# Optimization experiments

Measured on AMD Instinct MI355X. Metric: run time of the kernel, lower is better.

## Reference

```python
import jax, jax.numpy as jnp
import numpy as np

N_NODES = 100000
N_EDGES = 1600000
F_IN = 512    # args.in_channels (original node feature dim)
F_GNN = 128   # GCNConv output / 'in_channels' ctor arg
HID = 64
Z_DIM = 64
N_GRAPHS = 512


def setup_inputs() -> dict:
    key = jax.random.key(0)
    ks = jax.random.split(key, 20)
    x = jax.random.normal(ks[0], (N_NODES, F_IN), dtype=jnp.float32)
    edge_index = jax.random.randint(ks[1], (2, N_EDGES), 0, N_NODES)
    batch = jnp.sort(jax.random.randint(ks[2], (N_NODES,), 0, N_GRAPHS))
    eps = jax.random.normal(ks[3], (N_GRAPHS, Z_DIM), dtype=jnp.float32)

    def lin(k, fi, fo):
        # xavier_uniform weight, zero bias
        lim = float(np.sqrt(6.0 / (fi + fo)))
        W = jax.random.uniform(k, (fi, fo), minval=-lim, maxval=lim, dtype=jnp.float32)
        return W, jnp.zeros((fo,), dtype=jnp.float32)

    Wg, bg = lin(ks[4], F_IN, F_GNN)
    We1, be1 = lin(ks[5], 2 * F_GNN, HID)
    We2, be2 = lin(ks[6], HID, HID)
    We3, be3 = lin(ks[7], HID, 2 * Z_DIM)
    Wd1, bd1 = lin(ks[8], Z_DIM, HID)
    Wd2, bd2 = lin(ks[9], HID, HID)
    Wd3, bd3 = lin(ks[10], HID, F_GNN)
    return {"x": x, "edge_index": edge_index, "batch": batch, "eps": eps,
            "Wg": Wg, "bg": bg,
            "We1": We1, "be1": be1, "We2": We2, "be2": be2, "We3": We3, "be3": be3,
            "Wd1": Wd1, "bd1": bd1, "Wd2": Wd2, "bd2": bd2, "Wd3": Wd3, "bd3": bd3}


def _gcn_conv(x, edge_index, Wg, bg):
    # PyG GCNConv: add self-loops, symmetric deg normalization, linear-then-aggregate
    n = x.shape[0]
    loops = jnp.arange(n)
    src = jnp.concatenate([edge_index[0], loops])
    dst = jnp.concatenate([edge_index[1], loops])
    deg = jax.ops.segment_sum(jnp.ones_like(dst, dtype=x.dtype), dst, num_segments=n)
    dinv = jnp.where(deg > 0, jax.lax.rsqrt(jnp.maximum(deg, 1.0)), 0.0)
    norm = dinv[src] * dinv[dst]              # [E+N]
    xw = x @ Wg                               # [N, F_GNN]
    msg = xw[src] * norm[:, None]             # gather + scale: [E+N, F_GNN]
    agg = jax.ops.segment_sum(msg, dst, num_segments=n)
    return agg + bg


def _forward(x, edge_index, batch, eps,
             Wg, bg, We1, be1, We2, be2, We3, be3,
             Wd1, bd1, Wd2, bd2, Wd3, bd3):
    n = x.shape[0]
    g = eps.shape[0]
    # single GNN layer (num_layers=1, JK='last'); dropout omitted (eval determinism)
    node_x = jax.nn.relu(_gcn_conv(x, edge_index, Wg, bg))  # [N, F_GNN]
    # global mean / max pool by graph id
    ones = jnp.ones((n,), dtype=node_x.dtype)
    cnt = jax.ops.segment_sum(ones, batch, num_segments=g)
    mean_p = jax.ops.segment_sum(node_x, batch, num_segments=g) / jnp.maximum(cnt, 1.0)[:, None]
    max_p = jax.ops.segment_max(node_x, batch, num_segments=g)
    graph_x = jnp.concatenate([mean_p, max_p], axis=1)      # [G, 2*F_GNN]
    # gaussian encoder MLP
    t = jax.nn.elu(graph_x @ We1 + be1)
    t = jnp.tanh(t @ We2 + be2)
    ml = t @ We3 + be3
    mu, logvar = jnp.split(ml, 2, axis=1)
    # reparameterise (note: module returns stddev in the 'logvar' slot)
    stddev = 1e-6 + jax.nn.softplus(logvar)
    z = mu + eps * stddev
    # bernoulli decoder MLP
    d = jnp.tanh(z @ Wd1 + bd1)
    d = jax.nn.elu(d @ Wd2 + bd2)
    y = jax.nn.sigmoid(d @ Wd3 + bd3)
    y = jnp.clip(y, 1e-8, 1.0 - 1e-8)
    return mu, stddev, y


def reference(x, edge_index, batch, eps,
              Wg, bg, We1, be1, We2, be2, We3, be3,
              Wd1, bd1, Wd2, bd2, Wd3, bd3):
    return _forward(x, edge_index, batch, eps,
                    Wg, bg, We1, be1, We2, be2, We3, be3,
                    Wd1, bd1, Wd2, bd2, Wd3, bd3)
```

## Files before the change

kernel.cpp:

```cpp
#include <hip/hip_runtime.h>
#include <hip/hip_bf16.h>
#include <math.h>

#define N_NODES 100000
#define N_EDGES 1600000
#define F_IN 512
#define F_GNN 128
#define HID 64
#define Z_DIM 64
#define N_GRAPHS 512
#define N_REGIONS 196
#define REGION_CAP 10240

typedef __attribute__((ext_vector_type(8))) short short8;
typedef __attribute__((ext_vector_type(4))) float f32x4;

__device__ __forceinline__ float eluf(float v) { return v > 0.f ? v : expm1f(v); }
__device__ __forceinline__ float softplusf(float v) {
  return fmaxf(v, 0.f) + log1pf(expf(-fabsf(v)));
}
__device__ __forceinline__ float sigmoidf(float v) { return 1.f / (1.f + expf(-v)); }

__device__ __forceinline__ unsigned short f2bf(float f) {
  unsigned int u = __float_as_uint(f);
  u = (u + 0x7fffu + ((u >> 16) & 1u)) >> 16;
  return (unsigned short)u;
}
__device__ __forceinline__ unsigned int f2bf2(float a, float b) {
  __hip_bfloat162 h = __float22bfloat162_rn(make_float2(a, b));
  unsigned int u;
  __builtin_memcpy(&u, &h, 4);
  return u;
}
__device__ __forceinline__ float bf_lo(unsigned int u) { return __uint_as_float(u << 16); }
__device__ __forceinline__ float bf_hi(unsigned int u) { return __uint_as_float(u & 0xffff0000u); }

__device__ __forceinline__ int lower_bound_i(const int* __restrict__ a, int n, int v) {
  int lo = 0, hi = n;
  while (lo < hi) {
    int mid = (lo + hi) >> 1;
    if (a[mid] < v) lo = mid + 1; else hi = mid;
  }
  return lo;
}

__global__ void k_wg(const float* __restrict__ Wg, unsigned short* __restrict__ WgT,
                     int* __restrict__ rcnt) {
  int i = blockIdx.x * 256 + threadIdx.x;
  if (blockIdx.x == 0) rcnt[threadIdx.x] = 0;
  int n = i >> 9, k = i & 511;
  WgT[i] = f2bf(Wg[k * F_GNN + n]);
}

__global__ __launch_bounds__(256) void k_rcount(const int* __restrict__ ei,
                                                int* __restrict__ rcnt) {
  __shared__ int lh[256];
  const int b = blockIdx.x, t = threadIdx.x;
  lh[t] = 0;
  __syncthreads();
#pragma unroll
  for (int j = 0; j < 8; j++) {
    int e = b * 2048 + t + 256 * j;
    if (e < N_EDGES) atomicAdd(&lh[ei[N_EDGES + e] >> 9], 1);
  }
  __syncthreads();
  if (t < N_REGIONS && lh[t] > 0) atomicAdd(&rcnt[t], lh[t]);
}

__global__ __launch_bounds__(256) void k_rscan(int* __restrict__ rcnt,
                                               int* __restrict__ rbase) {
  __shared__ int s[256];
  int t = threadIdx.x;
  s[t] = (t < N_REGIONS) ? rcnt[t] : 0;
  __syncthreads();
#pragma unroll
  for (int d = 1; d < 256; d <<= 1) {
    int v = (t >= d) ? s[t - d] : 0;
    __syncthreads();
    s[t] += v;
    __syncthreads();
  }
  int excl = (t > 0) ? s[t - 1] : 0;
  rbase[t] = excl;
  rcnt[t] = excl;
  if (t == 255) rbase[N_REGIONS] = s[255];
}

__global__ __launch_bounds__(256) void k_bucket(
    const int* __restrict__ ei, int* __restrict__ cursor_r,
    uint2* __restrict__ pairs) {
  __shared__ int lhist[256];
  __shared__ int lofs[256];
  __shared__ int lcur[256];
  __shared__ int gbase[256];
  __shared__ int sc[256];
  __shared__ uint2 lpairs[4096];

  const int b = blockIdx.x, t = threadIdx.x;
  const int e0 = b * 4096;
  const int n_b = min(4096, N_EDGES - e0);

  lhist[t] = 0;
  lcur[t] = 0;
  __syncthreads();

  int srcv[16], dstv[16];
#pragma unroll
  for (int j = 0; j < 16; j++) {
    int e = e0 + t + 256 * j;
    if (e < N_EDGES) {
      srcv[j] = ei[e];
      dstv[j] = ei[N_EDGES + e];
      atomicAdd(&lhist[dstv[j] >> 9], 1);
    } else {
      dstv[j] = -1;
    }
  }
  __syncthreads();

  sc[t] = lhist[t];
  __syncthreads();
#pragma unroll
  for (int d = 1; d < 256; d <<= 1) {
    int v = (t >= d) ? sc[t - d] : 0;
    __syncthreads();
    sc[t] += v;
    __syncthreads();
  }
  lofs[t] = (t > 0) ? sc[t - 1] : 0;
  if (t < N_REGIONS && lhist[t] > 0) gbase[t] = atomicAdd(&cursor_r[t], lhist[t]);
  __syncthreads();

#pragma unroll
  for (int j = 0; j < 16; j++) {
    if (dstv[j] >= 0) {
      int r = dstv[j] >> 9;
      int pos = lofs[r] + atomicAdd(&lcur[r], 1);
      lpairs[pos] = make_uint2((unsigned)srcv[j], (unsigned)dstv[j]);
    }
  }
  __syncthreads();

  for (int i = t; i < n_b; i += 256) {
    int lo = 0, hi = N_REGIONS;
    while (hi - lo > 1) {
      int mid = (lo + hi) >> 1;
      if (lofs[mid] <= i) lo = mid; else hi = mid;
    }
    pairs[gbase[lo] + (i - lofs[lo])] = lpairs[i];
  }
}

__global__ __launch_bounds__(256) void k_region(
    const uint2* __restrict__ pairs, const int* __restrict__ rbase,
    int* __restrict__ off, float* __restrict__ dinv, int* __restrict__ csr_src) {
  __shared__ int nh[512];
  __shared__ int sofs[512];
  __shared__ int sc[256];
  __shared__ int ncur[512];
  __shared__ int cbuf[REGION_CAP];

  const int r = blockIdx.x, t = threadIdx.x;
  const int base = rbase[r];
  const int cnt = rbase[r + 1] - base;

  nh[t] = 0;
  nh[t + 256] = 0;
  __syncthreads();

  for (int i = t; i < cnt; i += 256) {
    uint2 p = pairs[base + i];
    atomicAdd(&nh[p.y & 511], 1);
  }
  __syncthreads();

  int a0 = nh[2 * t], a1 = nh[2 * t + 1];
  sc[t] = a0 + a1;
  __syncthreads();
#pragma unroll
  for (int d = 1; d < 256; d <<= 1) {
    int v = (t >= d) ? sc[t - d] : 0;
    __syncthreads();
    sc[t] += v;
    __syncthreads();
  }
  int excl = (t > 0) ? sc[t - 1] : 0;
  sofs[2 * t] = excl;
  sofs[2 * t + 1] = excl + a0;

  const int node0 = r << 9;
  int n0 = node0 + 2 * t;
  if (n0 < N_NODES)     { off[n0] = base + excl;      dinv[n0] = rsqrtf(1.f + (float)a0); }
  if (n0 + 1 < N_NODES) { off[n0 + 1] = base + excl + a0; dinv[n0 + 1] = rsqrtf(1.f + (float)a1); }
  if (r == N_REGIONS - 1 && t == 0) off[N_NODES] = N_EDGES;

  ncur[t] = 0;
  ncur[t + 256] = 0;
  __syncthreads();

  for (int i = t; i < cnt; i += 256) {
    uint2 p = pairs[base + i];
    int d = (int)p.y & 511;
    int lpos = sofs[d] + atomicAdd(&ncur[d], 1);
    if (lpos < REGION_CAP) cbuf[lpos] = (int)p.x;
  }
  __syncthreads();
  for (int i = t; i < cnt; i += 256) csr_src[base + i] = cbuf[i];
}

__global__ __launch_bounds__(256) void k_gemm(
    const float* __restrict__ x, const unsigned short* __restrict__ WgT,
    const float* __restrict__ dinv, unsigned short* __restrict__ sxw) {
  __shared__ unsigned short As[128][32];
  __shared__ unsigned short Bs[128][32];

  const int t = threadIdx.x;
  const int lane15 = t & 15;
  const int quad = (t & 63) >> 4;
  const int wave = t >> 6;
  const int wm = (wave & 1) * 64;
  const int wn = (wave >> 1) * 64;
  const int row0 = blockIdx.x * 128;

  f32x4 acc[4][4];
#pragma unroll
  for (int mi = 0; mi < 4; mi++)
#pragma unroll
    for (int ni = 0; ni < 4; ni++) acc[mi][ni] = (f32x4){0.f, 0.f, 0.f, 0.f};

  float4 ga[4];
  uint4 gb[2];
  auto load_tile = [&](int k0) {
#pragma unroll
    for (int i = 0; i < 4; i++) {
      int f = t + 256 * i;
      int r = f >> 3, c4 = f & 7;
      int gr = row0 + r;
      if (gr >= N_NODES) gr = N_NODES - 1;
      ga[i] = *(const float4*)&x[(size_t)gr * F_IN + k0 + c4 * 4];
    }
#pragma unroll
    for (int i = 0; i < 2; i++) {
      int f = t + 256 * i;
      int r = f >> 2, c = f & 3;
      gb[i] = *(const uint4*)&WgT[r * F_IN + k0 + c * 8];
    }
  };

  load_tile(0);
#pragma unroll 1
  for (int kt = 0; kt < 16; kt++) {
    __syncthreads();
#pragma unroll
    for (int i = 0; i < 4; i++) {
      int f = t + 256 * i;
      int r = f >> 3, c4 = f & 7;
      unsigned int u0 = f2bf2(ga[i].x, ga[i].y);
      unsigned int u1 = f2bf2(ga[i].z, ga[i].w);
      *(uint2*)&As[r][c4 * 4] = make_uint2(u0, u1);
    }
#pragma unroll
    for (int i = 0; i < 2; i++) {
      int f = t + 256 * i;
      int r = f >> 2, c = f & 3;
      *(uint4*)&Bs[r][c * 8] = gb[i];
    }
    __syncthreads();
    if (kt < 15) load_tile((kt + 1) * 32);

    short8 afr[4], bfr[4];
#pragma unroll
    for (int mi = 0; mi < 4; mi++)
      afr[mi] = *(const short8*)&As[wm + mi * 16 + lane15][quad * 8];
#pragma unroll
    for (int ni = 0; ni < 4; ni++)
      bfr[ni] = *(const short8*)&Bs[wn + ni * 16 + lane15][quad * 8];
#pragma unroll
    for (int mi = 0; mi < 4; mi++)
#pragma unroll
      for (int ni = 0; ni < 4; ni++)
        acc[mi][ni] = __builtin_amdgcn_mfma_f32_16x16x32_bf16(
            bfr[ni], afr[mi], acc[mi][ni], 0, 0, 0);
  }

#pragma unroll
  for (int mi = 0; mi < 4; mi++) {
    int gm = row0 + wm + mi * 16 + lane15;
    if (gm < N_NODES) {
      float s = dinv[gm];
#pragma unroll
      for (int ni = 0; ni < 4; ni++) {
        int gn = wn + ni * 16 + quad * 4;
        unsigned int u0 = f2bf2(acc[mi][ni][0] * s, acc[mi][ni][1] * s);
        unsigned int u1 = f2bf2(acc[mi][ni][2] * s, acc[mi][ni][3] * s);
        *(uint2*)&sxw[(size_t)gm * F_GNN + gn] = make_uint2(u0, u1);
      }
    }
  }
}

__global__ __launch_bounds__(1024) void k_aggpool(
    const unsigned short* __restrict__ sxw, const int* __restrict__ off,
    const int* __restrict__ csr_src, const float* __restrict__ dinv,
    const float* __restrict__ bg, const int* __restrict__ batch,
    float* __restrict__ gx) {
  __shared__ float2 ssum[16][64];
  __shared__ float2 smax[16][64];
  __shared__ int sse[2];
  const int g = blockIdx.x;
  const int t = threadIdx.x;
  const int wv = t >> 6;
  const int lane = t & 63;

  if (t == 0) sse[0] = lower_bound_i(batch, N_NODES, g);
  if (t == 64) sse[1] = lower_bound_i(batch, N_NODES, g + 1);
  __syncthreads();
  const int start = sse[0], end = sse[1];

  const unsigned int* S = (const unsigned int*)sxw;
  float2 b = ((const float2*)bg)[lane];
  float2 ps = make_float2(0.f, 0.f);
  float2 pm = make_float2(0.f, 0.f);

  for (int node = start + wv; node < end; node += 16) {
    unsigned int u = S[(size_t)node * 64 + lane];
    float sx = bf_lo(u), sy = bf_hi(u);
    int e = off[node];
    int e1 = off[node + 1];
    for (; e + 7 < e1; e += 8) {
      int s0 = csr_src[e + 0], s1 = csr_src[e + 1];
      int s2 = csr_src[e + 2], s3 = csr_src[e + 3];
      int s4 = csr_src[e + 4], s5 = csr_src[e + 5];
      int s6 = csr_src[e + 6], s7 = csr_src[e + 7];
      unsigned int v0 = S[(size_t)s0 * 64 + lane];
      unsigned int v1 = S[(size_t)s1 * 64 + lane];
      unsigned int v2 = S[(size_t)s2 * 64 + lane];
      unsigned int v3 = S[(size_t)s3 * 64 + lane];
      unsigned int v4 = S[(size_t)s4 * 64 + lane];
      unsigned int v5 = S[(size_t)s5 * 64 + lane];
      unsigned int v6 = S[(size_t)s6 * 64 + lane];
      unsigned int v7 = S[(size_t)s7 * 64 + lane];
      sx += bf_lo(v0) + bf_lo(v1) + bf_lo(v2) + bf_lo(v3)
          + bf_lo(v4) + bf_lo(v5) + bf_lo(v6) + bf_lo(v7);
      sy += bf_hi(v0) + bf_hi(v1) + bf_hi(v2) + bf_hi(v3)
          + bf_hi(v4) + bf_hi(v5) + bf_hi(v6) + bf_hi(v7);
    }
    for (; e < e1; e++) {
      unsigned int v0 = S[(size_t)csr_src[e] * 64 + lane];
      sx += bf_lo(v0);
      sy += bf_hi(v0);
    }
    float di = dinv[node];
    float rx = fmaxf(fmaf(sx, di, b.x), 0.f);
    float ry = fmaxf(fmaf(sy, di, b.y), 0.f);
    ps.x += rx; ps.y += ry;
    pm.x = fmaxf(pm.x, rx); pm.y = fmaxf(pm.y, ry);
  }

  ssum[wv][lane] = ps;
  smax[wv][lane] = pm;
  __syncthreads();
  if (t < 64) {
    float2 s = ssum[0][t];
    float2 m = smax[0][t];
#pragma unroll
    for (int h = 1; h < 16; h++) {
      s.x += ssum[h][t].x; s.y += ssum[h][t].y;
      m.x = fmaxf(m.x, smax[h][t].x); m.y = fmaxf(m.y, smax[h][t].y);
    }
    float ic = 1.f / fmaxf((float)(end - start), 1.f);
    gx[g * 256 + 2 * t] = s.x * ic;
    gx[g * 256 + 2 * t + 1] = s.y * ic;
    gx[g * 256 + 128 + 2 * t] = m.x;
    gx[g * 256 + 129 + 2 * t] = m.y;
  }
}

__global__ __launch_bounds__(64) void k_mlp(
    const float* __restrict__ gx, const float* __restrict__ eps,
    const float* __restrict__ We1, const float* __restrict__ be1,
    const float* __restrict__ We2, const float* __restrict__ be2,
    const float* __restrict__ We3, const float* __restrict__ be3,
    const float* __restrict__ Wd1, const float* __restrict__ bd1,
    const float* __restrict__ Wd2, const float* __restrict__ bd2,
    const float* __restrict__ Wd3, const float* __restrict__ bd3,
    float* __restrict__ out) {
  __shared__ float row[256];
  __shared__ float t1[64], t2[64], zz[64], d1[64], d2[64];
  int g = blockIdx.x;
  int j = threadIdx.x;

#pragma unroll
  for (int i = 0; i < 4; i++) row[j + 64 * i] = gx[g * 256 + j + 64 * i];
  __syncthreads();

  float s = be1[j];
#pragma unroll 4
  for (int k = 0; k < 256; k++) s = fmaf(row[k], We1[k * 64 + j], s);
  t1[j] = eluf(s);
  __syncthreads();

  s = be2[j];
#pragma unroll 4
  for (int k = 0; k < 64; k++) s = fmaf(t1[k], We2[k * 64 + j], s);
  t2[j] = tanhf(s);
  __syncthreads();

  float m = be3[j], lv = be3[64 + j];
#pragma unroll 4
  for (int k = 0; k < 64; k++) {
    float tv = t2[k];
    m = fmaf(tv, We3[k * 128 + j], m);
    lv = fmaf(tv, We3[k * 128 + 64 + j], lv);
  }
  float sd = 1e-6f + softplusf(lv);
  float z = fmaf(eps[g * 64 + j], sd, m);
  out[g * 64 + j] = m;
  out[32768 + g * 64 + j] = sd;
  zz[j] = z;
  __syncthreads();

  s = bd1[j];
#pragma unroll 4
  for (int k = 0; k < 64; k++) s = fmaf(zz[k], Wd1[k * 64 + j], s);
  d1[j] = tanhf(s);
  __syncthreads();

  s = bd2[j];
#pragma unroll 4
  for (int k = 0; k < 64; k++) s = fmaf(d1[k], Wd2[k * 64 + j], s);
  d2[j] = eluf(s);
  __syncthreads();

  float y0 = bd3[j], y1 = bd3[64 + j];
#pragma unroll 4
  for (int k = 0; k < 64; k++) {
    float dv = d2[k];
    y0 = fmaf(dv, Wd3[k * 128 + j], y0);
    y1 = fmaf(dv, Wd3[k * 128 + 64 + j], y1);
  }
  y0 = fminf(fmaxf(sigmoidf(y0), 1e-8f), 1.f - 1e-8f);
  y1 = fminf(fmaxf(sigmoidf(y1), 1e-8f), 1.f - 1e-8f);
  out[65536 + g * 128 + j] = y0;
  out[65536 + g * 128 + 64 + j] = y1;
}

extern "C" void kernel_launch(void* const* d_in, const int* in_sizes, int n_in,
                              void* d_out, int out_size, void* d_ws, size_t ws_size,
                              hipStream_t stream) {
  const float* x     = (const float*)d_in[0];
  const int*   ei    = (const int*)d_in[1];
  const int*   batch = (const int*)d_in[2];
  const float* eps   = (const float*)d_in[3];
  const float* Wg    = (const float*)d_in[4];
  const float* bg    = (const float*)d_in[5];
  const float* We1   = (const float*)d_in[6];
  const float* be1   = (const float*)d_in[7];
  const float* We2   = (const float*)d_in[8];
  const float* be2   = (const float*)d_in[9];
  const float* We3   = (const float*)d_in[10];
  const float* be3   = (const float*)d_in[11];
  const float* Wd1   = (const float*)d_in[12];
  const float* bd1   = (const float*)d_in[13];
  const float* Wd2   = (const float*)d_in[14];
  const float* bd2   = (const float*)d_in[15];
  const float* Wd3   = (const float*)d_in[16];
  const float* bd3   = (const float*)d_in[17];
  float* out = (float*)d_out;

  int*            rbase    = (int*)d_ws;
  int*            cursor_r = rbase + 256;
  int*            off      = cursor_r + 256;
  float*          dinv     = (float*)(off + 102656);
  int*            csr_src  = (int*)(dinv + 102400);
  uint2*          pairs    = (uint2*)(csr_src + 1600128);
  unsigned short* WgT      = (unsigned short*)(pairs + 1600000);
  unsigned short* sxw      = WgT + 65536;
  float*          gx       = (float*)(sxw + 12800000);

  k_wg<<<(F_IN * F_GNN) / 256, 256, 0, stream>>>(Wg, WgT, cursor_r);
  k_rcount<<<(N_EDGES + 2047) / 2048, 256, 0, stream>>>(ei, cursor_r);
  k_rscan<<<1, 256, 0, stream>>>(cursor_r, rbase);
  k_bucket<<<(N_EDGES + 4095) / 4096, 256, 0, stream>>>(ei, cursor_r, pairs);
  k_region<<<N_REGIONS, 256, 0, stream>>>(pairs, rbase, off, dinv, csr_src);
  k_gemm<<<(N_NODES + 127) / 128, 256, 0, stream>>>(x, WgT, dinv, sxw);
  k_aggpool<<<N_GRAPHS, 1024, 0, stream>>>(sxw, off, csr_src, dinv, bg, batch, gx);
  k_mlp<<<N_GRAPHS, 64, 0, stream>>>(gx, eps, We1, be1, We2, be2, We3, be3,
                                     Wd1, bd1, Wd2, bd2, Wd3, bd3, out);
}
```

Measured before the change: 559.4 us.

## Vectorize edge loads, widen preprocessing blocks, split edges across half-waves in aggregation

The Wg transpose moves into the region-count kernel, with a tiny zeroing kernel added in its place, and region counting and bucketing now read edge indices as int4. Bucketing and region build run 512-thread blocks, so the region scan becomes a single-element-per-thread 512 scan. In the aggregation-pool kernel each half-wave processes alternate neighbours with 8-byte loads covering four features, and the halves are combined with a cross-lane shuffle. The goal is more memory-level parallelism and fewer load instructions in the gather-heavy aggregation, plus fewer small launches. In exchange it adds shuffles and changes the workspace offsets.

```diff
diff --git a/kernel.cpp b/kernel.cpp
--- a/kernel.cpp
+++ b/kernel.cpp
@@ -44,24 +44,32 @@
   return lo;
 }
 
-__global__ void k_wg(const float* __restrict__ Wg, unsigned short* __restrict__ WgT,
-                     int* __restrict__ rcnt) {
-  int i = blockIdx.x * 256 + threadIdx.x;
-  if (blockIdx.x == 0) rcnt[threadIdx.x] = 0;
-  int n = i >> 9, k = i & 511;
-  WgT[i] = f2bf(Wg[k * F_GNN + n]);
-}
-
-__global__ __launch_bounds__(256) void k_rcount(const int* __restrict__ ei,
-                                                int* __restrict__ rcnt) {
+__global__ __launch_bounds__(256) void k_z(int* __restrict__ rcnt) {
+  rcnt[threadIdx.x] = 0;
+}
+
+__global__ __launch_bounds__(256) void k_rcount(
+    const int* __restrict__ ei, int* __restrict__ rcnt,
+    const float* __restrict__ Wg, unsigned short* __restrict__ WgT) {
   __shared__ int lh[256];
   const int b = blockIdx.x, t = threadIdx.x;
+  if (b < 256) {
+    int i = b * 256 + t;
+    int n = i >> 9, k = i & 511;
+    WgT[i] = f2bf(Wg[k * F_GNN + n]);
+  }
   lh[t] = 0;
   __syncthreads();
 #pragma unroll
-  for (int j = 0; j < 8; j++) {
-    int e = b * 2048 + t + 256 * j;
-    if (e < N_EDGES) atomicAdd(&lh[ei[N_EDGES + e] >> 9], 1);
+  for (int jj = 0; jj < 4; jj++) {
+    int e = b * 4096 + jj * 1024 + 4 * t;
+    if (e < N_EDGES) {
+      int4 d4 = *(const int4*)&ei[N_EDGES + e];
+      atomicAdd(&lh[d4.x >> 9], 1);
+      atomicAdd(&lh[d4.y >> 9], 1);
+      atomicAdd(&lh[d4.z >> 9], 1);
+      atomicAdd(&lh[d4.w >> 9], 1);
+    }
   }
   __syncthreads();
   if (t < N_REGIONS && lh[t] > 0) atomicAdd(&rcnt[t], lh[t]);
@@ -86,7 +94,7 @@
   if (t == 255) rbase[N_REGIONS] = s[255];
 }
 
-__global__ __launch_bounds__(256) void k_bucket(
+__global__ __launch_bounds__(512) void k_bucket(
     const int* __restrict__ ei, int* __restrict__ cursor_r,
     uint2* __restrict__ pairs) {
   __shared__ int lhist[256];
@@ -100,39 +108,45 @@
   const int e0 = b * 4096;
   const int n_b = min(4096, N_EDGES - e0);
 
-  lhist[t] = 0;
-  lcur[t] = 0;
-  __syncthreads();
-
-  int srcv[16], dstv[16];
-#pragma unroll
-  for (int j = 0; j < 16; j++) {
-    int e = e0 + t + 256 * j;
+  if (t < 256) { lhist[t] = 0; lcur[t] = 0; }
+  __syncthreads();
+
+  int srcv[8], dstv[8];
+#pragma unroll
+  for (int jj = 0; jj < 2; jj++) {
+    int e = e0 + jj * 2048 + 4 * t;
     if (e < N_EDGES) {
-      srcv[j] = ei[e];
-      dstv[j] = ei[N_EDGES + e];
-      atomicAdd(&lhist[dstv[j] >> 9], 1);
+      int4 s4 = *(const int4*)&ei[e];
+      int4 d4 = *(const int4*)&ei[N_EDGES + e];
+      srcv[4 * jj + 0] = s4.x; dstv[4 * jj + 0] = d4.x;
+      srcv[4 * jj + 1] = s4.y; dstv[4 * jj + 1] = d4.y;
+      srcv[4 * jj + 2] = s4.z; dstv[4 * jj + 2] = d4.z;
+      srcv[4 * jj + 3] = s4.w; dstv[4 * jj + 3] = d4.w;
+      atomicAdd(&lhist[d4.x >> 9], 1);
+      atomicAdd(&lhist[d4.y >> 9], 1);
+      atomicAdd(&lhist[d4.z >> 9], 1);
+      atomicAdd(&lhist[d4.w >> 9], 1);
     } else {
-      dstv[j] = -1;
-    }
-  }
-  __syncthreads();
-
-  sc[t] = lhist[t];
+      dstv[4 * jj + 0] = dstv[4 * jj + 1] = dstv[4 * jj + 2] = dstv[4 * jj + 3] = -1;
+    }
+  }
+  __syncthreads();
+
+  if (t < 256) sc[t] = lhist[t];
   __syncthreads();
 #pragma unroll
   for (int d = 1; d < 256; d <<= 1) {
-    int v = (t >= d) ? sc[t - d] : 0;
-    __syncthreads();
-    sc[t] += v;
-    __syncthreads();
-  }
-  lofs[t] = (t > 0) ? sc[t - 1] : 0;
+    int v = (t < 256 && t >= d) ? sc[t - d] : 0;
+    __syncthreads();
+    if (t < 256) sc[t] += v;
+    __syncthreads();
+  }
+  if (t < 256) lofs[t] = (t > 0) ? sc[t - 1] : 0;
   if (t < N_REGIONS && lhist[t] > 0) gbase[t] = atomicAdd(&cursor_r[t], lhist[t]);
   __syncthreads();
 
 #pragma unroll
-  for (int j = 0; j < 16; j++) {
+  for (int j = 0; j < 8; j++) {
     if (dstv[j] >= 0) {
       int r = dstv[j] >> 9;
       int pos = lofs[r] + atomicAdd(&lcur[r], 1);
@@ -141,7 +155,7 @@
   }
   __syncthreads();
 
-  for (int i = t; i < n_b; i += 256) {
+  for (int i = t; i < n_b; i += 512) {
     int lo = 0, hi = N_REGIONS;
     while (hi - lo > 1) {
       int mid = (lo + hi) >> 1;
@@ -151,12 +165,12 @@
   }
 }
 
-__global__ __launch_bounds__(256) void k_region(
+__global__ __launch_bounds__(512) void k_region(
     const uint2* __restrict__ pairs, const int* __restrict__ rbase,
     int* __restrict__ off, float* __restrict__ dinv, int* __restrict__ csr_src) {
   __shared__ int nh[512];
   __shared__ int sofs[512];
-  __shared__ int sc[256];
+  __shared__ int s[512];
   __shared__ int ncur[512];
   __shared__ int cbuf[REGION_CAP];
 
@@ -165,47 +179,44 @@
   const int cnt = rbase[r + 1] - base;
 
   nh[t] = 0;
-  nh[t + 256] = 0;
-  __syncthreads();
-
-  for (int i = t; i < cnt; i += 256) {
+  ncur[t] = 0;
+  __syncthreads();
+
+  for (int i = t; i < cnt; i += 512) {
     uint2 p = pairs[base + i];
     atomicAdd(&nh[p.y & 511], 1);
   }
   __syncthreads();
 
-  int a0 = nh[2 * t], a1 = nh[2 * t + 1];
-  sc[t] = a0 + a1;
-  __syncthreads();
-#pragma unroll
-  for (int d = 1; d < 256; d <<= 1) {
-    int v = (t >= d) ? sc[t - d] : 0;
-    __syncthreads();
-    sc[t] += v;
-    __syncthreads();
-  }
-  int excl = (t > 0) ? sc[t - 1] : 0;
-  sofs[2 * t] = excl;
-  sofs[2 * t + 1] = excl + a0;
-
-  const int node0 = r << 9;
-  int n0 = node0 + 2 * t;
-  if (n0 < N_NODES)     { off[n0] = base + excl;      dinv[n0] = rsqrtf(1.f + (float)a0); }
-  if (n0 + 1 < N_NODES) { off[n0 + 1] = base + excl + a0; dinv[n0 + 1] = rsqrtf(1.f + (float)a1); }
+  int a = nh[t];
+  s[t] = a;
+  __syncthreads();
+#pragma unroll
+  for (int d = 1; d < 512; d <<= 1) {
+    int v = (t >= d) ? s[t - d] : 0;
+    __syncthreads();
+    s[t] += v;
+    __syncthreads();
+  }
+  int excl = (t > 0) ? s[t - 1] : 0;
+  sofs[t] = excl;
+
+  const int node = (r << 9) + t;
+  if (node < N_NODES) {
+    off[node] = base + excl;
+    dinv[node] = rsqrtf(1.f + (float)a);
+  }
   if (r == N_REGIONS - 1 && t == 0) off[N_NODES] = N_EDGES;
-
-  ncur[t] = 0;
-  ncur[t + 256] = 0;
-  __syncthreads();
-
-  for (int i = t; i < cnt; i += 256) {
+  __syncthreads();
+
+  for (int i = t; i < cnt; i += 512) {
     uint2 p = pairs[base + i];
     int d = (int)p.y & 511;
     int lpos = sofs[d] + atomicAdd(&ncur[d], 1);
     if (lpos < REGION_CAP) cbuf[lpos] = (int)p.x;
   }
   __syncthreads();
-  for (int i = t; i < cnt; i += 256) csr_src[base + i] = cbuf[i];
+  for (int i = t; i < cnt; i += 512) csr_src[base + i] = cbuf[i];
 }
 
 __global__ __launch_bounds__(256) void k_gemm(
@@ -304,75 +315,97 @@
     const int* __restrict__ csr_src, const float* __restrict__ dinv,
     const float* __restrict__ bg, const int* __restrict__ batch,
     float* __restrict__ gx) {
-  __shared__ float2 ssum[16][64];
-  __shared__ float2 smax[16][64];
+  __shared__ float4 ssum[16][32];
+  __shared__ float4 smax[16][32];
   __shared__ int sse[2];
   const int g = blockIdx.x;
   const int t = threadIdx.x;
   const int wv = t >> 6;
   const int lane = t & 63;
+  const int h = lane >> 5;
+  const int c = lane & 31;
 
   if (t == 0) sse[0] = lower_bound_i(batch, N_NODES, g);
   if (t == 64) sse[1] = lower_bound_i(batch, N_NODES, g + 1);
   __syncthreads();
   const int start = sse[0], end = sse[1];
 
-  const unsigned int* S = (const unsigned int*)sxw;
-  float2 b = ((const float2*)bg)[lane];
-  float2 ps = make_float2(0.f, 0.f);
-  float2 pm = make_float2(0.f, 0.f);
+  const uint2* S2 = (const uint2*)sxw;
+  float4 bb = ((const float4*)bg)[c];
+  float ps0 = 0.f, ps1 = 0.f, ps2 = 0.f, ps3 = 0.f;
+  float pm0 = 0.f, pm1 = 0.f, pm2 = 0.f, pm3 = 0.f;
 
   for (int node = start + wv; node < end; node += 16) {
-    unsigned int u = S[(size_t)node * 64 + lane];
-    float sx = bf_lo(u), sy = bf_hi(u);
+    float sx0 = 0.f, sx1 = 0.f, sx2 = 0.f, sx3 = 0.f;
     int e = off[node];
-    int e1 = off[node + 1];
+    const int e1 = off[node + 1];
     for (; e + 7 < e1; e += 8) {
       int s0 = csr_src[e + 0], s1 = csr_src[e + 1];
       int s2 = csr_src[e + 2], s3 = csr_src[e + 3];
       int s4 = csr_src[e + 4], s5 = csr_src[e + 5];
       int s6 = csr_src[e + 6], s7 = csr_src[e + 7];
-      unsigned int v0 = S[(size_t)s0 * 64 + lane];
-      unsigned int v1 = S[(size_t)s1 * 64 + lane];
-      unsigned int v2 = S[(size_t)s2 * 64 + lane];
-      unsigned int v3 = S[(size_t)s3 * 64 + lane];
-      unsigned int v4 = S[(size_t)s4 * 64 + lane];
-      unsigned int v5 = S[(size_t)s5 * 64 + lane];
-      unsigned int v6 = S[(size_t)s6 * 64 + lane];
-      unsigned int v7 = S[(size_t)s7 * 64 + lane];
-      sx += bf_lo(v0) + bf_lo(v1) + bf_lo(v2) + bf_lo(v3)
-          + bf_lo(v4) + bf_lo(v5) + bf_lo(v6) + bf_lo(v7);
-      sy += bf_hi(v0) + bf_hi(v1) + bf_hi(v2) + bf_hi(v3)
-          + bf_hi(v4) + bf_hi(v5) + bf_hi(v6) + bf_hi(v7);
-    }
-    for (; e < e1; e++) {
-      unsigned int v0 = S[(size_t)csr_src[e] * 64 + lane];
-      sx += bf_lo(v0);
-      sy += bf_hi(v0);
-    }
+      uint2 v0 = S2[(size_t)(h ? s1 : s0) * 32 + c];
+      uint2 v1 = S2[(size_t)(h ? s3 : s2) * 32 + c];
+      uint2 v2 = S2[(size_t)(h ? s5 : s4) * 32 + c];
+      uint2 v3 = S2[(size_t)(h ? s7 : s6) * 32 + c];
+      sx0 += bf_lo(v0.x) + bf_lo(v1.x) + bf_lo(v2.x) + bf_lo(v3.x);
+      sx1 += bf_hi(v0.x) + bf_hi(v1.x) + bf_hi(v2.x) + bf_hi(v3.x);
+      sx2 += bf_lo(v0.y) + bf_lo(v1.y) + bf_lo(v2.y) + bf_lo(v3.y);
+      sx3 += bf_hi(v0.y) + bf_hi(v1.y) + bf_hi(v2.y) + bf_hi(v3.y);
+    }
+    for (; e + 1 < e1; e += 2) {
+      int sa = csr_src[e], sb = csr_src[e + 1];
+      uint2 v = S2[(size_t)(h ? sb : sa) * 32 + c];
+      sx0 += bf_lo(v.x); sx1 += bf_hi(v.x);
+      sx2 += bf_lo(v.y); sx3 += bf_hi(v.y);
+    }
+    if (e < e1 && h == 0) {
+      uint2 v = S2[(size_t)csr_src[e] * 32 + c];
+      sx0 += bf_lo(v.x); sx1 += bf_hi(v.x);
+      sx2 += bf_lo(v.y); sx3 += bf_hi(v.y);
+    }
+    sx0 += __shfl_xor(sx0, 32);
+    sx1 += __shfl_xor(sx1, 32);
+    sx2 += __shfl_xor(sx2, 32);
+    sx3 += __shfl_xor(sx3, 32);
+    uint2 sv = S2[(size_t)node * 32 + c];
+    sx0 += bf_lo(sv.x); sx1 += bf_hi(sv.x);
+    sx2 += bf_lo(sv.y); sx3 += bf_hi(sv.y);
+
     float di = dinv[node];
-    float rx = fmaxf(fmaf(sx, di, b.x), 0.f);
-    float ry = fmaxf(fmaf(sy, di, b.y), 0.f);
-    ps.x += rx; ps.y += ry;
-    pm.x = fmaxf(pm.x, rx); pm.y = fmaxf(pm.y, ry);
-  }
-
-  ssum[wv][lane] = ps;
-  smax[wv][lane] = pm;
-  __syncthreads();
-  if (t < 64) {
-    float2 s = ssum[0][t];
-    float2 m = smax[0][t];
-#pragma unroll
-    for (int h = 1; h < 16; h++) {
-      s.x += ssum[h][t].x; s.y += ssum[h][t].y;
-      m.x = fmaxf(m.x, smax[h][t].x); m.y = fmaxf(m.y, smax[h][t].y);
+    float r0 = fmaxf(fmaf(sx0, di, bb.x), 0.f);
+    float r1 = fmaxf(fmaf(sx1, di, bb.y), 0.f);
+    float r2 = fmaxf(fmaf(sx2, di, bb.z), 0.f);
+    float r3 = fmaxf(fmaf(sx3, di, bb.w), 0.f);
+    ps0 += r0; ps1 += r1; ps2 += r2; ps3 += r3;
+    pm0 = fmaxf(pm0, r0); pm1 = fmaxf(pm1, r1);
+    pm2 = fmaxf(pm2, r2); pm3 = fmaxf(pm3, r3);
+  }
+
+  if (h == 0) {
+    ssum[wv][c] = make_float4(ps0, ps1, ps2, ps3);
+    smax[wv][c] = make_float4(pm0, pm1, pm2, pm3);
+  }
+  __syncthreads();
+  if (t < 32) {
+    float4 s = ssum[0][t];
+    float4 m = smax[0][t];
+#pragma unroll
+    for (int hh = 1; hh < 16; hh++) {
+      float4 a = ssum[hh][t], b2 = smax[hh][t];
+      s.x += a.x; s.y += a.y; s.z += a.z; s.w += a.w;
+      m.x = fmaxf(m.x, b2.x); m.y = fmaxf(m.y, b2.y);
+      m.z = fmaxf(m.z, b2.z); m.w = fmaxf(m.w, b2.w);
     }
     float ic = 1.f / fmaxf((float)(end - start), 1.f);
-    gx[g * 256 + 2 * t] = s.x * ic;
-    gx[g * 256 + 2 * t + 1] = s.y * ic;
-    gx[g * 256 + 128 + 2 * t] = m.x;
-    gx[g * 256 + 129 + 2 * t] = m.y;
+    gx[g * 256 + 4 * t + 0] = s.x * ic;
+    gx[g * 256 + 4 * t + 1] = s.y * ic;
+    gx[g * 256 + 4 * t + 2] = s.z * ic;
+    gx[g * 256 + 4 * t + 3] = s.w * ic;
+    gx[g * 256 + 128 + 4 * t + 0] = m.x;
+    gx[g * 256 + 128 + 4 * t + 1] = m.y;
+    gx[g * 256 + 128 + 4 * t + 2] = m.z;
+    gx[g * 256 + 128 + 4 * t + 3] = m.w;
   }
 }
 
@@ -468,21 +501,21 @@
   const float* bd3   = (const float*)d_in[17];
   float* out = (float*)d_out;
 
-  int*            rbase    = (int*)d_ws;
-  int*            cursor_r = rbase + 256;
-  int*            off      = cursor_r + 256;
-  float*          dinv     = (float*)(off + 102656);
-  int*            csr_src  = (int*)(dinv + 102400);
-  uint2*          pairs    = (uint2*)(csr_src + 1600128);
-  unsigned short* WgT      = (unsigned short*)(pairs + 1600000);
-  unsigned short* sxw      = WgT + 65536;
-  float*          gx       = (float*)(sxw + 12800000);
-
-  k_wg<<<(F_IN * F_GNN) / 256, 256, 0, stream>>>(Wg, WgT, cursor_r);
-  k_rcount<<<(N_EDGES + 2047) / 2048, 256, 0, stream>>>(ei, cursor_r);
-  k_rscan<<<1, 256, 0, stream>>>(cursor_r, rbase);
-  k_bucket<<<(N_EDGES + 4095) / 4096, 256, 0, stream>>>(ei, cursor_r, pairs);
-  k_region<<<N_REGIONS, 256, 0, stream>>>(pairs, rbase, off, dinv, csr_src);
+  int*            rbase   = (int*)d_ws;
+  int*            rcnt    = rbase + 256;
+  int*            off     = rcnt + 256;
+  float*          dinv    = (float*)(off + 100608);
+  int*            csr_src = (int*)(dinv + 100352);
+  uint2*          pairs   = (uint2*)(csr_src + 1600000);
+  unsigned short* WgT     = (unsigned short*)(pairs + 1600000);
+  unsigned short* sxw     = WgT + 65536;
+  float*          gx      = (float*)(sxw + 12800000);
+
+  k_z<<<1, 256, 0, stream>>>(rcnt);
+  k_rcount<<<(N_EDGES + 4095) / 4096, 256, 0, stream>>>(ei, rcnt, Wg, WgT);
+  k_rscan<<<1, 256, 0, stream>>>(rcnt, rbase);
+  k_bucket<<<(N_EDGES + 4095) / 4096, 512, 0, stream>>>(ei, rcnt, pairs);
+  k_region<<<N_REGIONS, 512, 0, stream>>>(pairs, rbase, off, dinv, csr_src);
   k_gemm<<<(N_NODES + 127) / 128, 256, 0, stream>>>(x, WgT, dinv, sxw);
   k_aggpool<<<N_GRAPHS, 1024, 0, stream>>>(sxw, off, csr_src, dinv, bg, batch, gx);
   k_mlp<<<N_GRAPHS, 64, 0, stream>>>(gx, eps, We1, be1, We2, be2, We3, be3,
```

Result: faster. 528.5 us (-5.5%).
